# Kernel tuning notes

Measured on AMD Instinct MI355X. Metric: run time of the kernel, lower is better.

The kernel has to match this reference:

```python
import jax, jax.numpy as jnp
import numpy as np
from jax import lax

NPOINT = 1024
NSAMPLE = 32
RADIUS = 0.6
BN_EPS = 1e-5


def square_distance(src, dst):
    # src (B,S,3), dst (B,N,3) -> (B,S,N) squared distances
    d = -2.0 * jnp.einsum('bsc,bnc->bsn', src, dst)
    d = d + jnp.sum(src ** 2, -1)[:, :, None]
    d = d + jnp.sum(dst ** 2, -1)[:, None, :]
    return d


def farthest_point_sample(xyz, npoint):
    B, N, _ = xyz.shape
    bidx = jnp.arange(B)

    def step(carry, _):
        distance, farthest = carry
        centroid = xyz[bidx, farthest]                      # (B,3)
        dist = jnp.sum((xyz - centroid[:, None, :]) ** 2, -1)  # (B,N)
        distance = jnp.minimum(distance, dist)
        new_far = jnp.argmax(distance, -1)
        return (distance, new_far), farthest

    init = (jnp.full((B, N), 1e10, xyz.dtype), jnp.zeros((B,), jnp.int32))
    _, idxs = lax.scan(step, init, None, length=npoint)
    return idxs.T                                            # (B,npoint)


def ball_query(xyz, new_xyz, radius, nsample):
    B, N, _ = xyz.shape
    sqr = square_distance(new_xyz, xyz)                      # (B,S,N)
    idx = jnp.where(sqr <= radius ** 2, jnp.arange(N)[None, None, :], N)
    idx = jnp.sort(idx, axis=-1)[:, :, :nsample]             # (B,S,K)
    first = idx[:, :, :1]
    return jnp.where(idx == N, first, idx)


def gather2(points, idx):
    # points (B,N,C), idx (B,S) -> (B,S,C)
    return jax.vmap(lambda p, i: p[i])(points, idx)


def gather3(points, idx):
    # points (B,N,C), idx (B,S,K) -> (B,S,K,C)
    return jax.vmap(lambda p, i: p[i])(points, idx)


def sa_forward(xyz, features, params):
    fps_idx = lax.stop_gradient(farthest_point_sample(xyz, NPOINT))
    new_xyz = gather2(xyz, fps_idx)                          # (B,S,3)
    idx = lax.stop_gradient(ball_query(xyz, new_xyz, RADIUS, NSAMPLE))
    grouped_xyz = gather3(xyz, idx) - new_xyz[:, :, None, :] # (B,S,K,3)
    grouped_feat = gather3(features.transpose(0, 2, 1), idx) # (B,S,K,C)
    g = jnp.concatenate([grouped_xyz, grouped_feat], -1)     # (B,S,K,C+3)
    g = g.transpose(0, 3, 2, 1)                              # (B,Cin,K,S)
    for w, b, ga, be in params:
        g = jnp.einsum('oc,bcks->boks', w, g) + b[None, :, None, None]
        mu = jnp.mean(g, axis=(0, 2, 3), keepdims=True)
        var = jnp.var(g, axis=(0, 2, 3), keepdims=True)
        g = ga[None, :, None, None] * (g - mu) * lax.rsqrt(var + BN_EPS) \
            + be[None, :, None, None]
        g = jax.nn.relu(g)
    new_features = jnp.max(g, axis=2)                        # (B,Cout,S)
    return new_xyz, new_features


def setup_inputs() -> dict:
    key = jax.random.key(0)
    ks = jax.random.split(key, 8)
    B, N, C = 16, 4096, 128
    cin = C + 3
    mlp = [128, 128, 256]
    inp = {
        'xyz': jax.random.normal(ks[0], (B, N, 3), jnp.float32),
        'features': jax.random.normal(ks[1], (B, C, N), jnp.float32),
    }
    prev = cin
    for i, out in enumerate(mlp):
        inp[f'w{i}'] = jax.random.normal(ks[2 + i], (out, prev), jnp.float32) * 0.05
        inp[f'b{i}'] = jnp.zeros((out,), jnp.float32)
        inp[f'gamma{i}'] = jnp.ones((out,), jnp.float32)
        inp[f'beta{i}'] = jnp.zeros((out,), jnp.float32)
        prev = out
    return inp


def reference(xyz, features, w0, b0, gamma0, beta0, w1, b1, gamma1, beta1,
              w2, b2, gamma2, beta2):
    params = [(w0, b0, gamma0, beta0), (w1, b1, gamma1, beta1),
              (w2, b2, gamma2, beta2)]
    return sa_forward(xyz, features, params)
```

## Files before the change

### kernel.cpp

```cpp
#include <hip/hip_runtime.h>

#define B_ 16
#define N_ 4096
#define S_ 1024
#define K_ 32
#define PITCH2 136
#define PITCH1 168

typedef unsigned long long u64;
typedef short bf16x8 __attribute__((ext_vector_type(8)));
typedef unsigned short u16x8 __attribute__((ext_vector_type(8)));
typedef float f32x4 __attribute__((ext_vector_type(4)));
typedef float f32x2 __attribute__((ext_vector_type(2)));

__device__ __forceinline__ unsigned short f2bf(float f) {
  unsigned u = __float_as_uint(f);
  unsigned r = (u + 0x7FFFu + ((u >> 16) & 1u)) >> 16;
  return (unsigned short)r;
}
__device__ __forceinline__ float bf2f(unsigned short h) {
  return __uint_as_float(((unsigned)h) << 16);
}

#define DPP_MAX(v, ctrl)                                                        \
  {                                                                             \
    int _t = __builtin_amdgcn_update_dpp(__float_as_int(v), __float_as_int(v),  \
                                         ctrl, 0xf, 0xf, false);                \
    v = fmaxf(v, __int_as_float(_t));                                           \
  }

__global__ __launch_bounds__(512) void k_front(
    const float* __restrict__ xyz, float* __restrict__ new_xyz,
    const float* __restrict__ feat, unsigned short* __restrict__ featT,
    const float* __restrict__ w0, const float* __restrict__ w1,
    const float* __restrict__ w2, unsigned short* __restrict__ wbf0,
    unsigned short* __restrict__ wbf1, unsigned short* __restrict__ wbf2,
    float* __restrict__ stats) {
  __shared__ __align__(16) float smem[N_ * 4 + S_ + 64];
  int blk = blockIdx.x, t = threadIdx.x;

  if (blk < 16) {
#pragma clang fp contract(off)
#if __has_builtin(__builtin_amdgcn_s_setprio)
    __builtin_amdgcn_s_setprio(3);
#endif
    float4* pts = (float4*)smem;
    int* idxs = (int*)(smem + N_ * 4);
    u64* swk = (u64*)(smem + N_ * 4 + S_);
    int b = blk;
    const float* base = xyz + (size_t)b * N_ * 3;
    for (int i = t; i < N_; i += 512)
      pts[i] = make_float4(base[i * 3], base[i * 3 + 1], base[i * 3 + 2], 0.0f);
    if (t == 0) idxs[0] = 0;
    __syncthreads();
    f32x2 px[4], py[4], pz[4], pd[4];
    int i0 = t * 8;
    #pragma unroll
    for (int j = 0; j < 4; ++j) {
      float4 p0 = pts[i0 + 2 * j], p1 = pts[i0 + 2 * j + 1];
      px[j] = (f32x2){p0.x, p1.x};
      py[j] = (f32x2){p0.y, p1.y};
      pz[j] = (f32x2){p0.z, p1.z};
      pd[j] = (f32x2){1e10f, 1e10f};
    }
    int cur = 0;
    for (int it = 0; it < S_; ++it) {
      float4 c = pts[cur];
      f32x2 c2x = (f32x2){c.x, c.x}, c2y = (f32x2){c.y, c.y}, c2z = (f32x2){c.z, c.z};
      float bestv = -1.0f; int besti = 0;
      #pragma unroll
      for (int j = 0; j < 4; ++j) {
        f32x2 dx = px[j] - c2x;
        f32x2 dy = py[j] - c2y;
        f32x2 dz = pz[j] - c2z;
        f32x2 d = (dx * dx + dy * dy) + dz * dz;
        f32x2 dm = __builtin_elementwise_min(pd[j], d);
        pd[j] = dm;
        if (dm.x > bestv) { bestv = dm.x; besti = 2 * j; }
        if (dm.y > bestv) { bestv = dm.y; besti = 2 * j + 1; }
      }
      float v = bestv;
      DPP_MAX(v, 0x111);
      DPP_MAX(v, 0x112);
      DPP_MAX(v, 0x114);
      DPP_MAX(v, 0x118);
      DPP_MAX(v, 0x142);
      DPP_MAX(v, 0x143);
      float wmax = __int_as_float(__builtin_amdgcn_readlane(__float_as_int(v), 63));
      u64 mask = __ballot(bestv == wmax);
      int owner = __ffsll((long long)mask) - 1;
      int widx = __builtin_amdgcn_readlane(i0 + besti, owner);
      if ((t & 63) == 0)
        swk[(it & 1) * 8 + (t >> 6)] =
            ((u64)__float_as_uint(wmax) << 32) | (unsigned)(4095 - widx);
      __syncthreads();
      const u64* kk = swk + (it & 1) * 8;
      u64 k0 = kk[0];
      #pragma unroll
      for (int w = 1; w < 8; ++w) if (kk[w] > k0) k0 = kk[w];
      cur = 4095 - (int)(unsigned)(k0 & 0xFFFFFFFFull);
      if (t == 0 && it + 1 < S_) idxs[it + 1] = cur;
    }
    __syncthreads();
    for (int i = t; i < S_; i += 512) {
      float4 v = pts[idxs[i]];
      size_t o = ((size_t)b * S_ + i) * 3;
      new_xyz[o] = v.x; new_xyz[o + 1] = v.y; new_xyz[o + 2] = v.z;
    }
  } else if (blk < 32) {
    int id = (blk - 16) * 512 + t;
    const int st = 16 * 512;
    for (int i = id; i < 32768; i += st) stats[i] = 0.0f;
    for (int i = id; i < 128 * 160; i += st) {
      int n = i / 160, k = i - n * 160;
      float v = (k < 128) ? w0[n * 131 + 3 + k] : (k < 131) ? w0[n * 131 + k - 128] : 0.0f;
      wbf0[i] = f2bf(v);
    }
    for (int i = id; i < 128 * 128; i += st) wbf1[i] = f2bf(w1[i]);
    for (int i = id; i < 256 * 128; i += st) wbf2[i] = f2bf(w2[i]);
  } else {
    float (*tile)[33] = (float(*)[33])smem;
    int blk2 = blk - 32;
    int n0 = (blk2 & 127) * 32;
    int c0 = ((blk2 >> 7) & 3) * 32;
    int b = blk2 >> 9;
    int tx = t & 31, ty = t >> 5;
    #pragma unroll
    for (int j = 0; j < 32; j += 16)
      tile[ty + j][tx] = feat[((size_t)b * 128 + c0 + ty + j) * N_ + n0 + tx];
    __syncthreads();
    #pragma unroll
    for (int j = 0; j < 32; j += 16)
      featT[((size_t)b * N_ + n0 + ty + j) * 128 + c0 + tx] = f2bf(tile[tx][ty + j]);
  }
}

__global__ __launch_bounds__(256) void k_ballq(const float* __restrict__ xyz,
                                               const float* __restrict__ new_xyz,
                                               int* __restrict__ ball_idx) {
  int b = blockIdx.y;
  int s = blockIdx.x * 4 + (threadIdx.x >> 6);
  int lane = threadIdx.x & 63;
  const float* pb = xyz + (size_t)b * N_ * 3;
  size_t q = (size_t)b * S_ + s;
  float qx = new_xyz[q * 3], qy = new_xyz[q * 3 + 1], qz = new_xyz[q * 3 + 2];
  float sq = __fadd_rn(__fadd_rn(__fmul_rn(qx, qx), __fmul_rn(qy, qy)), __fmul_rn(qz, qz));
  int* out = ball_idx + q * K_;
  int total = 0;
  int first_idx = -1;
  for (int basei = 0; basei < N_; basei += 64) {
    int i = basei + lane;
    float fx = pb[i * 3], fy = pb[i * 3 + 1], fz = pb[i * 3 + 2];
    float dot = __fmul_rn(qx, fx);
    dot = __fadd_rn(dot, __fmul_rn(qy, fy));
    dot = __fadd_rn(dot, __fmul_rn(qz, fz));
    float sd = __fadd_rn(__fadd_rn(__fmul_rn(fx, fx), __fmul_rn(fy, fy)), __fmul_rn(fz, fz));
    float dist = __fadd_rn(__fadd_rn(__fmul_rn(-2.0f, dot), sq), sd);
    bool within = (dist <= 0.36f);
    u64 m = __ballot(within);
    if (first_idx < 0 && m) first_idx = basei + __ffsll((long long)m) - 1;
    if (within) {
      int pos = total + __popcll(m & ((1ull << lane) - 1ull));
      if (pos < K_) out[pos] = i;
    }
    total += (int)__popcll(m);
    if (total >= K_) break;
  }
  if (total < K_) {
    int k2 = total + lane;
    if (k2 < K_) out[k2] = first_idx;
  }
}

#define MFMA(a, b, c) __builtin_amdgcn_mfma_f32_16x16x32_bf16(a, b, c, 0, 0, 0)

__global__ __launch_bounds__(256) void k_layer1(
    const float* __restrict__ xyz, const float* __restrict__ new_xyz,
    const unsigned short* __restrict__ featT, const int* __restrict__ ball_idx,
    const unsigned short* __restrict__ wbf0, const float* __restrict__ b0,
    unsigned short* __restrict__ y, float* __restrict__ stats) {
  __shared__ __align__(16) unsigned short Wl[128 * PITCH1];
  __shared__ float sbias[128];
  int bb = blockIdx.y, s0 = blockIdx.x * 4, t = threadIdx.x;
  int w = t >> 6, L = t & 63, lm = L & 15, lg = L >> 4;
  size_t qg = (size_t)bb * S_ + s0 + w;

  int p0 = ball_idx[qg * K_ + lm];
  int p1 = ball_idx[qg * K_ + 16 + lm];
  const unsigned short* f0 = featT + ((size_t)bb * N_ + p0) * 128;
  const unsigned short* f1 = featT + ((size_t)bb * N_ + p1) * 128;
  bf16x8 a0[5], a1[5];
  #pragma unroll
  for (int kt = 0; kt < 4; ++kt) {
    a0[kt] = *(const bf16x8*)(f0 + kt * 32 + lg * 8);
    a1[kt] = *(const bf16x8*)(f1 + kt * 32 + lg * 8);
  }
  a0[4] = (bf16x8){0, 0, 0, 0, 0, 0, 0, 0};
  a1[4] = (bf16x8){0, 0, 0, 0, 0, 0, 0, 0};
  if (lg == 0) {
    float nx = new_xyz[qg * 3], ny = new_xyz[qg * 3 + 1], nz = new_xyz[qg * 3 + 2];
    const float* pp0 = xyz + ((size_t)bb * N_ + p0) * 3;
    const float* pp1 = xyz + ((size_t)bb * N_ + p1) * 3;
    a0[4][0] = (short)f2bf(pp0[0] - nx);
    a0[4][1] = (short)f2bf(pp0[1] - ny);
    a0[4][2] = (short)f2bf(pp0[2] - nz);
    a1[4][0] = (short)f2bf(pp1[0] - nx);
    a1[4][1] = (short)f2bf(pp1[1] - ny);
    a1[4][2] = (short)f2bf(pp1[2] - nz);
  }
  {
    int n = t >> 1, h = t & 1;
    const uint4* wr = (const uint4*)(wbf0 + n * 160 + h * 80);
    uint4* wl = (uint4*)(Wl + n * PITCH1 + h * 80);
    #pragma unroll
    for (int i = 0; i < 10; ++i) wl[i] = wr[i];
    if (t < 128) sbias[t] = b0[t];
  }
  __syncthreads();
  f32x4 acc[2][8];
  #pragma unroll
  for (int mi = 0; mi < 2; ++mi)
    #pragma unroll
    for (int nt = 0; nt < 8; ++nt) acc[mi][nt] = (f32x4){0.f, 0.f, 0.f, 0.f};
  #pragma unroll
  for (int kt = 0; kt < 5; ++kt) {
    int ko = kt * 32 + lg * 8;
    bf16x8 bv[8];
    #pragma unroll
    for (int nt = 0; nt < 8; ++nt)
      bv[nt] = *(const bf16x8*)&Wl[(nt * 16 + lm) * PITCH1 + ko];
    #pragma unroll
    for (int nt = 0; nt < 8; ++nt) {
      acc[0][nt] = MFMA(a0[kt], bv[nt], acc[0][nt]);
      acc[1][nt] = MFMA(a1[kt], bv[nt], acc[1][nt]);
    }
  }
  int slot = blockIdx.x & 31;
  #pragma unroll
  for (int nt = 0; nt < 8; ++nt) {
    int col = nt * 16 + lm;
    float bo = sbias[col];
    float s1 = 0.f, s2 = 0.f;
    #pragma unroll
    for (int mi = 0; mi < 2; ++mi)
      #pragma unroll
      for (int r = 0; r < 4; ++r) {
        float yv = acc[mi][nt][r] + bo;
        s1 += yv; s2 += yv * yv;
        int ks = mi * 16 + lg * 4 + r;
        y[(qg * K_ + ks) * 128 + col] = f2bf(yv);
      }
    s1 += __shfl_xor(s1, 16); s2 += __shfl_xor(s2, 16);
    s1 += __shfl_xor(s1, 32); s2 += __shfl_xor(s2, 32);
    if (lg == 0) {
      atomicAdd(stats + ((size_t)slot * 128 + col) * 2, s1);
      atomicAdd(stats + ((size_t)slot * 128 + col) * 2 + 1, s2);
    }
  }
}

__global__ __launch_bounds__(256) void k_layer2(
    unsigned short* y, const float* __restrict__ stats,
    const float* __restrict__ gamma, const float* __restrict__ beta,
    const unsigned short* __restrict__ wbf1, const float* __restrict__ b1,
    float* __restrict__ stats2) {
  __shared__ __align__(16) unsigned short Wl[128 * PITCH2];
  __shared__ __align__(16) float sa[128], sd[128];
  __shared__ float sbias[128];
  int bb = blockIdx.y, s0 = blockIdx.x * 4, t = threadIdx.x;
  int w = t >> 6, L = t & 63, lm = L & 15, lg = L >> 4;
  size_t qg = (size_t)bb * S_ + s0 + w;

  const u16x8* yr0 = (const u16x8*)(y + (qg * K_ + lm) * 128);
  const u16x8* yr1 = (const u16x8*)(y + (qg * K_ + 16 + lm) * 128);
  u16x8 raw0[4], raw1[4];
  #pragma unroll
  for (int kt = 0; kt < 4; ++kt) { raw0[kt] = yr0[kt * 4 + lg]; raw1[kt] = yr1[kt * 4 + lg]; }

  if (t < 128) {
    float s1 = 0.0f, s2 = 0.0f;
    for (int sl = 0; sl < 32; ++sl) {
      s1 += stats[((size_t)sl * 128 + t) * 2];
      s2 += stats[((size_t)sl * 128 + t) * 2 + 1];
    }
    const float inv = 1.0f / 524288.0f;
    float mu = s1 * inv;
    float var = s2 * inv - mu * mu;
    float a = gamma[t] * rsqrtf(var + 1e-5f);
    sa[t] = a;
    sd[t] = beta[t] - a * mu;
    sbias[t] = b1[t];
  }
  {
    int n = t >> 1, h = t & 1;
    const uint4* wr = (const uint4*)(wbf1 + n * 128 + h * 64);
    uint4* wl = (uint4*)(Wl + n * PITCH2 + h * 64);
    #pragma unroll
    for (int i = 0; i < 8; ++i) wl[i] = wr[i];
  }
  __syncthreads();
  bf16x8 a0[4], a1[4];
  #pragma unroll
  for (int kt = 0; kt < 4; ++kt) {
    int c = kt * 32 + lg * 8;
    f32x4 A0 = *(const f32x4*)&sa[c], A1 = *(const f32x4*)&sa[c + 4];
    f32x4 D0 = *(const f32x4*)&sd[c], D1 = *(const f32x4*)&sd[c + 4];
    #pragma unroll
    for (int j = 0; j < 4; ++j) {
      a0[kt][j]     = (short)f2bf(fmaxf(A0[j] * bf2f(raw0[kt][j])     + D0[j], 0.f));
      a0[kt][j + 4] = (short)f2bf(fmaxf(A1[j] * bf2f(raw0[kt][j + 4]) + D1[j], 0.f));
      a1[kt][j]     = (short)f2bf(fmaxf(A0[j] * bf2f(raw1[kt][j])     + D0[j], 0.f));
      a1[kt][j + 4] = (short)f2bf(fmaxf(A1[j] * bf2f(raw1[kt][j + 4]) + D1[j], 0.f));
    }
  }
  f32x4 acc[2][8];
  #pragma unroll
  for (int mi = 0; mi < 2; ++mi)
    #pragma unroll
    for (int nt = 0; nt < 8; ++nt) acc[mi][nt] = (f32x4){0.f, 0.f, 0.f, 0.f};
  #pragma unroll
  for (int kt = 0; kt < 4; ++kt) {
    int ko = kt * 32 + lg * 8;
    bf16x8 bv[8];
    #pragma unroll
    for (int nt = 0; nt < 8; ++nt)
      bv[nt] = *(const bf16x8*)&Wl[(nt * 16 + lm) * PITCH2 + ko];
    #pragma unroll
    for (int nt = 0; nt < 8; ++nt) {
      acc[0][nt] = MFMA(a0[kt], bv[nt], acc[0][nt]);
      acc[1][nt] = MFMA(a1[kt], bv[nt], acc[1][nt]);
    }
  }
  int slot = blockIdx.x & 31;
  #pragma unroll
  for (int nt = 0; nt < 8; ++nt) {
    int col = nt * 16 + lm;
    float bo = sbias[col];
    float s1 = 0.f, s2 = 0.f;
    #pragma unroll
    for (int mi = 0; mi < 2; ++mi)
      #pragma unroll
      for (int r = 0; r < 4; ++r) {
        float yv = acc[mi][nt][r] + bo;
        s1 += yv; s2 += yv * yv;
        int ks = mi * 16 + lg * 4 + r;
        y[(qg * K_ + ks) * 128 + col] = f2bf(yv);
      }
    s1 += __shfl_xor(s1, 16); s2 += __shfl_xor(s2, 16);
    s1 += __shfl_xor(s1, 32); s2 += __shfl_xor(s2, 32);
    if (lg == 0) {
      atomicAdd(stats2 + ((size_t)slot * 128 + col) * 2, s1);
      atomicAdd(stats2 + ((size_t)slot * 128 + col) * 2 + 1, s2);
    }
  }
}

__global__ __launch_bounds__(256) void k_layer3(
    const unsigned short* __restrict__ y, const float* __restrict__ stats2,
    const float* __restrict__ gamma, const float* __restrict__ beta,
    const unsigned short* __restrict__ wbf2, const float* __restrict__ b2,
    unsigned short* __restrict__ ymax, unsigned short* __restrict__ ymin,
    float* __restrict__ stats3) {
  __shared__ __align__(16) unsigned short Wl[128 * PITCH2];
  __shared__ __align__(16) float sa[128], sd[128];
  __shared__ float sbias[128];
  int bb = blockIdx.y, s0 = blockIdx.x * 4, nh = blockIdx.z, t = threadIdx.x;
  int w = t >> 6, L = t & 63, lm = L & 15, lg = L >> 4;
  size_t qg = (size_t)bb * S_ + s0 + w;

  const u16x8* yr0 = (const u16x8*)(y + (qg * K_ + lm) * 128);
  const u16x8* yr1 = (const u16x8*)(y + (qg * K_ + 16 + lm) * 128);
  u16x8 raw0[4], raw1[4];
  #pragma unroll
  for (int kt = 0; kt < 4; ++kt) { raw0[kt] = yr0[kt * 4 + lg]; raw1[kt] = yr1[kt * 4 + lg]; }

  if (t < 128) {
    float s1 = 0.0f, s2 = 0.0f;
    for (int sl = 0; sl < 32; ++sl) {
      s1 += stats2[((size_t)sl * 128 + t) * 2];
      s2 += stats2[((size_t)sl * 128 + t) * 2 + 1];
    }
    const float inv = 1.0f / 524288.0f;
    float mu = s1 * inv;
    float var = s2 * inv - mu * mu;
    float a = gamma[t] * rsqrtf(var + 1e-5f);
    sa[t] = a;
    sd[t] = beta[t] - a * mu;
    sbias[t] = b2[nh * 128 + t];
  }
  {
    int n = t >> 1, h = t & 1;
    const uint4* wr = (const uint4*)(wbf2 + (size_t)(nh * 128 + n) * 128 + h * 64);
    uint4* wl = (uint4*)(Wl + n * PITCH2 + h * 64);
    #pragma unroll
    for (int i = 0; i < 8; ++i) wl[i] = wr[i];
  }
  __syncthreads();
  bf16x8 a0[4], a1[4];
  #pragma unroll
  for (int kt = 0; kt < 4; ++kt) {
    int c = kt * 32 + lg * 8;
    f32x4 A0 = *(const f32x4*)&sa[c], A1 = *(const f32x4*)&sa[c + 4];
    f32x4 D0 = *(const f32x4*)&sd[c], D1 = *(const f32x4*)&sd[c + 4];
    #pragma unroll
    for (int j = 0; j < 4; ++j) {
      a0[kt][j]     = (short)f2bf(fmaxf(A0[j] * bf2f(raw0[kt][j])     + D0[j], 0.f));
      a0[kt][j + 4] = (short)f2bf(fmaxf(A1[j] * bf2f(raw0[kt][j + 4]) + D1[j], 0.f));
      a1[kt][j]     = (short)f2bf(fmaxf(A0[j] * bf2f(raw1[kt][j])     + D0[j], 0.f));
      a1[kt][j + 4] = (short)f2bf(fmaxf(A1[j] * bf2f(raw1[kt][j + 4]) + D1[j], 0.f));
    }
  }
  f32x4 acc[2][8];
  #pragma unroll
  for (int mi = 0; mi < 2; ++mi)
    #pragma unroll
    for (int nt = 0; nt < 8; ++nt) acc[mi][nt] = (f32x4){0.f, 0.f, 0.f, 0.f};
  #pragma unroll
  for (int kt = 0; kt < 4; ++kt) {
    int ko = kt * 32 + lg * 8;
    bf16x8 bv[8];
    #pragma unroll
    for (int nt = 0; nt < 8; ++nt)
      bv[nt] = *(const bf16x8*)&Wl[(nt * 16 + lm) * PITCH2 + ko];
    #pragma unroll
    for (int nt = 0; nt < 8; ++nt) {
      acc[0][nt] = MFMA(a0[kt], bv[nt], acc[0][nt]);
      acc[1][nt] = MFMA(a1[kt], bv[nt], acc[1][nt]);
    }
  }
  int slot = blockIdx.x & 31;
  #pragma unroll
  for (int nt = 0; nt < 8; ++nt) {
    int col = nt * 16 + lm;
    int o = nh * 128 + col;
    float bo = sbias[col];
    float s1 = 0.f, s2 = 0.f, mx = -3.4e38f, mn = 3.4e38f;
    #pragma unroll
    for (int mi = 0; mi < 2; ++mi)
      #pragma unroll
      for (int r = 0; r < 4; ++r) {
        float yv = acc[mi][nt][r] + bo;
        s1 += yv; s2 += yv * yv;
        mx = fmaxf(mx, yv); mn = fminf(mn, yv);
      }
    s1 += __shfl_xor(s1, 16); s2 += __shfl_xor(s2, 16);
    s1 += __shfl_xor(s1, 32); s2 += __shfl_xor(s2, 32);
    mx = fmaxf(mx, __shfl_xor(mx, 16)); mx = fmaxf(mx, __shfl_xor(mx, 32));
    mn = fminf(mn, __shfl_xor(mn, 16)); mn = fminf(mn, __shfl_xor(mn, 32));
    if (lg == 0) {
      ymax[qg * 256 + o] = f2bf(mx);
      ymin[qg * 256 + o] = f2bf(mn);
      atomicAdd(stats3 + ((size_t)slot * 256 + o) * 2, s1);
      atomicAdd(stats3 + ((size_t)slot * 256 + o) * 2 + 1, s2);
    }
  }
}

__global__ __launch_bounds__(256) void k_final(const unsigned short* __restrict__ ymax,
                                               const unsigned short* __restrict__ ymin,
                                               const float* __restrict__ stats3,
                                               const float* __restrict__ gamma,
                                               const float* __restrict__ beta,
                                               float* __restrict__ out2) {
  __shared__ float tile[32][33];
  __shared__ float smA[32], smD[32];
  int b = blockIdx.z, o0 = blockIdx.y * 32, s0 = blockIdx.x * 32;
  int tx = threadIdx.x, ty = threadIdx.y;
  if (ty == 0) {
    int c = o0 + tx;
    float s1 = 0.0f, s2 = 0.0f;
    for (int sl = 0; sl < 32; ++sl) {
      s1 += stats3[((size_t)sl * 256 + c) * 2];
      s2 += stats3[((size_t)sl * 256 + c) * 2 + 1];
    }
    const float inv = 1.0f / 524288.0f;
    float mu = s1 * inv;
    float var = s2 * inv - mu * mu;
    float a = gamma[c] * rsqrtf(var + 1e-5f);
    smA[tx] = a;
    smD[tx] = beta[c] - a * mu;
  }
  __syncthreads();
  float a_rd = smA[tx];
  #pragma unroll
  for (int j = 0; j < 32; j += 8) {
    size_t src = ((size_t)b * S_ + s0 + ty + j) * 256 + o0 + tx;
    tile[ty + j][tx] = (a_rd >= 0.0f) ? bf2f(ymax[src]) : bf2f(ymin[src]);
  }
  __syncthreads();
  #pragma unroll
  for (int j = 0; j < 32; j += 8) {
    float a = smA[ty + j], dd = smD[ty + j];
    out2[((size_t)b * 256 + o0 + ty + j) * S_ + s0 + tx] = fmaxf(a * tile[tx][ty + j] + dd, 0.0f);
  }
}

extern "C" void kernel_launch(void* const* d_in, const int* in_sizes, int n_in,
                              void* d_out, int out_size, void* d_ws, size_t ws_size,
                              hipStream_t stream) {
  (void)in_sizes; (void)n_in; (void)out_size; (void)ws_size;
  const float* xyz  = (const float*)d_in[0];
  const float* feat = (const float*)d_in[1];
  const float* w0   = (const float*)d_in[2];
  const float* b0   = (const float*)d_in[3];
  const float* ga0  = (const float*)d_in[4];
  const float* be0  = (const float*)d_in[5];
  const float* w1   = (const float*)d_in[6];
  const float* b1   = (const float*)d_in[7];
  const float* ga1  = (const float*)d_in[8];
  const float* be1  = (const float*)d_in[9];
  const float* w2   = (const float*)d_in[10];
  const float* b2   = (const float*)d_in[11];
  const float* ga2  = (const float*)d_in[12];
  const float* be2  = (const float*)d_in[13];

  float* out_xyz  = (float*)d_out;
  float* out_feat = out_xyz + (size_t)B_ * S_ * 3;

  char* ws = (char*)d_ws;
  size_t off = 0;
  auto alloc = [&](size_t bytes) -> void* {
    void* p = ws + off;
    off += (bytes + 255) & ~(size_t)255;
    return p;
  };
  unsigned short* featT = (unsigned short*)alloc((size_t)B_ * N_ * 128 * 2);
  int*   ball  = (int*)alloc((size_t)B_ * S_ * K_ * 4);
  float* stats = (float*)alloc(32768 * 4);
  unsigned short* wbf0 = (unsigned short*)alloc(128 * 160 * 2);
  unsigned short* wbf1 = (unsigned short*)alloc(128 * 128 * 2);
  unsigned short* wbf2 = (unsigned short*)alloc(256 * 128 * 2);
  unsigned short* ymaxb = (unsigned short*)alloc((size_t)B_ * S_ * 256 * 2);
  unsigned short* yminb = (unsigned short*)alloc((size_t)B_ * S_ * 256 * 2);
  unsigned short* y = (unsigned short*)alloc((size_t)B_ * S_ * K_ * 128 * 2);

  k_front<<<16 + 16 + 8192, 512, 0, stream>>>(xyz, out_xyz, feat, featT,
                                              w0, w1, w2, wbf0, wbf1, wbf2, stats);
  k_ballq<<<dim3(256, 16), 256, 0, stream>>>(xyz, out_xyz, ball);
  k_layer1<<<dim3(256, 16), 256, 0, stream>>>(xyz, out_xyz, featT, ball, wbf0, b0, y, stats);
  k_layer2<<<dim3(256, 16), 256, 0, stream>>>(y, stats, ga0, be0, wbf1, b1, stats + 8192);
  k_layer3<<<dim3(256, 16, 2), 256, 0, stream>>>(y, stats + 8192, ga1, be1, wbf2, b2,
                                                 ymaxb, yminb, stats + 16384);
  k_final<<<dim3(32, 8, 16), dim3(32, 8), 0, stream>>>(ymaxb, yminb, stats + 16384,
                                                       ga2, be2, out_feat);
}
```

Measured before the change: 1.133 ms.

## Make MLP layer kernels persistent to amortize weight staging across tiles

The three MLP layer kernels become grid-stride persistent loops over 4096 tiles, launched with 768, 1024 and 512x2 blocks instead of one block per tile. Each block loads the bf16 weight matrix into LDS, and computes the BN scale/shift from the 32 stat slots, once, then reuses them for several tiles. This removes the repeated per-tile weight copy and stats reduction. The cost is fewer blocks in flight and no overlap between one tile's global loads and the previous tile's MFMA work.

```diff
diff --git a/kernel.cpp b/kernel.cpp
--- a/kernel.cpp
+++ b/kernel.cpp
@@ -173,6 +173,7 @@
 }
 
 #define MFMA(a, b, c) __builtin_amdgcn_mfma_f32_16x16x32_bf16(a, b, c, 0, 0, 0)
+#define NTILES 4096
 
 __global__ __launch_bounds__(256) void k_layer1(
     const float* __restrict__ xyz, const float* __restrict__ new_xyz,
@@ -181,33 +182,8 @@
     unsigned short* __restrict__ y, float* __restrict__ stats) {
   __shared__ __align__(16) unsigned short Wl[128 * PITCH1];
   __shared__ float sbias[128];
-  int bb = blockIdx.y, s0 = blockIdx.x * 4, t = threadIdx.x;
+  int t = threadIdx.x;
   int w = t >> 6, L = t & 63, lm = L & 15, lg = L >> 4;
-  size_t qg = (size_t)bb * S_ + s0 + w;
-
-  int p0 = ball_idx[qg * K_ + lm];
-  int p1 = ball_idx[qg * K_ + 16 + lm];
-  const unsigned short* f0 = featT + ((size_t)bb * N_ + p0) * 128;
-  const unsigned short* f1 = featT + ((size_t)bb * N_ + p1) * 128;
-  bf16x8 a0[5], a1[5];
-  #pragma unroll
-  for (int kt = 0; kt < 4; ++kt) {
-    a0[kt] = *(const bf16x8*)(f0 + kt * 32 + lg * 8);
-    a1[kt] = *(const bf16x8*)(f1 + kt * 32 + lg * 8);
-  }
-  a0[4] = (bf16x8){0, 0, 0, 0, 0, 0, 0, 0};
-  a1[4] = (bf16x8){0, 0, 0, 0, 0, 0, 0, 0};
-  if (lg == 0) {
-    float nx = new_xyz[qg * 3], ny = new_xyz[qg * 3 + 1], nz = new_xyz[qg * 3 + 2];
-    const float* pp0 = xyz + ((size_t)bb * N_ + p0) * 3;
-    const float* pp1 = xyz + ((size_t)bb * N_ + p1) * 3;
-    a0[4][0] = (short)f2bf(pp0[0] - nx);
-    a0[4][1] = (short)f2bf(pp0[1] - ny);
-    a0[4][2] = (short)f2bf(pp0[2] - nz);
-    a1[4][0] = (short)f2bf(pp1[0] - nx);
-    a1[4][1] = (short)f2bf(pp1[1] - ny);
-    a1[4][2] = (short)f2bf(pp1[2] - nz);
-  }
   {
     int n = t >> 1, h = t & 1;
     const uint4* wr = (const uint4*)(wbf0 + n * 160 + h * 80);
@@ -217,44 +193,74 @@
     if (t < 128) sbias[t] = b0[t];
   }
   __syncthreads();
-  f32x4 acc[2][8];
-  #pragma unroll
-  for (int mi = 0; mi < 2; ++mi)
-    #pragma unroll
-    for (int nt = 0; nt < 8; ++nt) acc[mi][nt] = (f32x4){0.f, 0.f, 0.f, 0.f};
-  #pragma unroll
-  for (int kt = 0; kt < 5; ++kt) {
-    int ko = kt * 32 + lg * 8;
-    bf16x8 bv[8];
-    #pragma unroll
-    for (int nt = 0; nt < 8; ++nt)
-      bv[nt] = *(const bf16x8*)&Wl[(nt * 16 + lm) * PITCH1 + ko];
+
+  for (int tile = blockIdx.x; tile < NTILES; tile += gridDim.x) {
+    int bb = tile >> 8;
+    int s0 = (tile & 255) * 4;
+    size_t qg = (size_t)bb * S_ + s0 + w;
+
+    int p0 = ball_idx[qg * K_ + lm];
+    int p1 = ball_idx[qg * K_ + 16 + lm];
+    const unsigned short* f0 = featT + ((size_t)bb * N_ + p0) * 128;
+    const unsigned short* f1 = featT + ((size_t)bb * N_ + p1) * 128;
+    bf16x8 a0[5], a1[5];
+    #pragma unroll
+    for (int kt = 0; kt < 4; ++kt) {
+      a0[kt] = *(const bf16x8*)(f0 + kt * 32 + lg * 8);
+      a1[kt] = *(const bf16x8*)(f1 + kt * 32 + lg * 8);
+    }
+    a0[4] = (bf16x8){0, 0, 0, 0, 0, 0, 0, 0};
+    a1[4] = (bf16x8){0, 0, 0, 0, 0, 0, 0, 0};
+    if (lg == 0) {
+      float nx = new_xyz[qg * 3], ny = new_xyz[qg * 3 + 1], nz = new_xyz[qg * 3 + 2];
+      const float* pp0 = xyz + ((size_t)bb * N_ + p0) * 3;
+      const float* pp1 = xyz + ((size_t)bb * N_ + p1) * 3;
+      a0[4][0] = (short)f2bf(pp0[0] - nx);
+      a0[4][1] = (short)f2bf(pp0[1] - ny);
+      a0[4][2] = (short)f2bf(pp0[2] - nz);
+      a1[4][0] = (short)f2bf(pp1[0] - nx);
+      a1[4][1] = (short)f2bf(pp1[1] - ny);
+      a1[4][2] = (short)f2bf(pp1[2] - nz);
+    }
+    f32x4 acc[2][8];
+    #pragma unroll
+    for (int mi = 0; mi < 2; ++mi)
+      #pragma unroll
+      for (int nt = 0; nt < 8; ++nt) acc[mi][nt] = (f32x4){0.f, 0.f, 0.f, 0.f};
+    #pragma unroll
+    for (int kt = 0; kt < 5; ++kt) {
+      int ko = kt * 32 + lg * 8;
+      bf16x8 bv[8];
+      #pragma unroll
+      for (int nt = 0; nt < 8; ++nt)
+        bv[nt] = *(const bf16x8*)&Wl[(nt * 16 + lm) * PITCH1 + ko];
+      #pragma unroll
+      for (int nt = 0; nt < 8; ++nt) {
+        acc[0][nt] = MFMA(a0[kt], bv[nt], acc[0][nt]);
+        acc[1][nt] = MFMA(a1[kt], bv[nt], acc[1][nt]);
+      }
+    }
+    int slot = tile & 31;
     #pragma unroll
     for (int nt = 0; nt < 8; ++nt) {
-      acc[0][nt] = MFMA(a0[kt], bv[nt], acc[0][nt]);
-      acc[1][nt] = MFMA(a1[kt], bv[nt], acc[1][nt]);
-    }
-  }
-  int slot = blockIdx.x & 31;
-  #pragma unroll
-  for (int nt = 0; nt < 8; ++nt) {
-    int col = nt * 16 + lm;
-    float bo = sbias[col];
-    float s1 = 0.f, s2 = 0.f;
-    #pragma unroll
-    for (int mi = 0; mi < 2; ++mi)
-      #pragma unroll
-      for (int r = 0; r < 4; ++r) {
-        float yv = acc[mi][nt][r] + bo;
-        s1 += yv; s2 += yv * yv;
-        int ks = mi * 16 + lg * 4 + r;
-        y[(qg * K_ + ks) * 128 + col] = f2bf(yv);
-      }
-    s1 += __shfl_xor(s1, 16); s2 += __shfl_xor(s2, 16);
-    s1 += __shfl_xor(s1, 32); s2 += __shfl_xor(s2, 32);
-    if (lg == 0) {
-      atomicAdd(stats + ((size_t)slot * 128 + col) * 2, s1);
-      atomicAdd(stats + ((size_t)slot * 128 + col) * 2 + 1, s2);
+      int col = nt * 16 + lm;
+      float bo = sbias[col];
+      float s1 = 0.f, s2 = 0.f;
+      #pragma unroll
+      for (int mi = 0; mi < 2; ++mi)
+        #pragma unroll
+        for (int r = 0; r < 4; ++r) {
+          float yv = acc[mi][nt][r] + bo;
+          s1 += yv; s2 += yv * yv;
+          int ks = mi * 16 + lg * 4 + r;
+          y[(qg * K_ + ks) * 128 + col] = f2bf(yv);
+        }
+      s1 += __shfl_xor(s1, 16); s2 += __shfl_xor(s2, 16);
+      s1 += __shfl_xor(s1, 32); s2 += __shfl_xor(s2, 32);
+      if (lg == 0) {
+        atomicAdd(stats + ((size_t)slot * 128 + col) * 2, s1);
+        atomicAdd(stats + ((size_t)slot * 128 + col) * 2 + 1, s2);
+      }
     }
   }
 }
@@ -267,16 +273,8 @@
   __shared__ __align__(16) unsigned short Wl[128 * PITCH2];
   __shared__ __align__(16) float sa[128], sd[128];
   __shared__ float sbias[128];
-  int bb = blockIdx.y, s0 = blockIdx.x * 4, t = threadIdx.x;
+  int t = threadIdx.x;
   int w = t >> 6, L = t & 63, lm = L & 15, lg = L >> 4;
-  size_t qg = (size_t)bb * S_ + s0 + w;
-
-  const u16x8* yr0 = (const u16x8*)(y + (qg * K_ + lm) * 128);
-  const u16x8* yr1 = (const u16x8*)(y + (qg * K_ + 16 + lm) * 128);
-  u16x8 raw0[4], raw1[4];
-  #pragma unroll
-  for (int kt = 0; kt < 4; ++kt) { raw0[kt] = yr0[kt * 4 + lg]; raw1[kt] = yr1[kt * 4 + lg]; }
-
   if (t < 128) {
     float s1 = 0.0f, s2 = 0.0f;
     for (int sl = 0; sl < 32; ++sl) {
@@ -299,58 +297,70 @@
     for (int i = 0; i < 8; ++i) wl[i] = wr[i];
   }
   __syncthreads();
-  bf16x8 a0[4], a1[4];
-  #pragma unroll
-  for (int kt = 0; kt < 4; ++kt) {
-    int c = kt * 32 + lg * 8;
-    f32x4 A0 = *(const f32x4*)&sa[c], A1 = *(const f32x4*)&sa[c + 4];
-    f32x4 D0 = *(const f32x4*)&sd[c], D1 = *(const f32x4*)&sd[c + 4];
-    #pragma unroll
-    for (int j = 0; j < 4; ++j) {
-      a0[kt][j]     = (short)f2bf(fmaxf(A0[j] * bf2f(raw0[kt][j])     + D0[j], 0.f));
-      a0[kt][j + 4] = (short)f2bf(fmaxf(A1[j] * bf2f(raw0[kt][j + 4]) + D1[j], 0.f));
-      a1[kt][j]     = (short)f2bf(fmaxf(A0[j] * bf2f(raw1[kt][j])     + D0[j], 0.f));
-      a1[kt][j + 4] = (short)f2bf(fmaxf(A1[j] * bf2f(raw1[kt][j + 4]) + D1[j], 0.f));
-    }
-  }
-  f32x4 acc[2][8];
-  #pragma unroll
-  for (int mi = 0; mi < 2; ++mi)
-    #pragma unroll
-    for (int nt = 0; nt < 8; ++nt) acc[mi][nt] = (f32x4){0.f, 0.f, 0.f, 0.f};
-  #pragma unroll
-  for (int kt = 0; kt < 4; ++kt) {
-    int ko = kt * 32 + lg * 8;
-    bf16x8 bv[8];
-    #pragma unroll
-    for (int nt = 0; nt < 8; ++nt)
-      bv[nt] = *(const bf16x8*)&Wl[(nt * 16 + lm) * PITCH2 + ko];
+
+  for (int tile = blockIdx.x; tile < NTILES; tile += gridDim.x) {
+    int bb = tile >> 8;
+    int s0 = (tile & 255) * 4;
+    size_t qg = (size_t)bb * S_ + s0 + w;
+
+    const u16x8* yr0 = (const u16x8*)(y + (qg * K_ + lm) * 128);
+    const u16x8* yr1 = (const u16x8*)(y + (qg * K_ + 16 + lm) * 128);
+    u16x8 raw0[4], raw1[4];
+    #pragma unroll
+    for (int kt = 0; kt < 4; ++kt) { raw0[kt] = yr0[kt * 4 + lg]; raw1[kt] = yr1[kt * 4 + lg]; }
+    bf16x8 a0[4], a1[4];
+    #pragma unroll
+    for (int kt = 0; kt < 4; ++kt) {
+      int c = kt * 32 + lg * 8;
+      f32x4 A0 = *(const f32x4*)&sa[c], A1 = *(const f32x4*)&sa[c + 4];
+      f32x4 D0 = *(const f32x4*)&sd[c], D1 = *(const f32x4*)&sd[c + 4];
+      #pragma unroll
+      for (int j = 0; j < 4; ++j) {
+        a0[kt][j]     = (short)f2bf(fmaxf(A0[j] * bf2f(raw0[kt][j])     + D0[j], 0.f));
+        a0[kt][j + 4] = (short)f2bf(fmaxf(A1[j] * bf2f(raw0[kt][j + 4]) + D1[j], 0.f));
+        a1[kt][j]     = (short)f2bf(fmaxf(A0[j] * bf2f(raw1[kt][j])     + D0[j], 0.f));
+        a1[kt][j + 4] = (short)f2bf(fmaxf(A1[j] * bf2f(raw1[kt][j + 4]) + D1[j], 0.f));
+      }
+    }
+    f32x4 acc[2][8];
+    #pragma unroll
+    for (int mi = 0; mi < 2; ++mi)
+      #pragma unroll
+      for (int nt = 0; nt < 8; ++nt) acc[mi][nt] = (f32x4){0.f, 0.f, 0.f, 0.f};
+    #pragma unroll
+    for (int kt = 0; kt < 4; ++kt) {
+      int ko = kt * 32 + lg * 8;
+      bf16x8 bv[8];
+      #pragma unroll
+      for (int nt = 0; nt < 8; ++nt)
+        bv[nt] = *(const bf16x8*)&Wl[(nt * 16 + lm) * PITCH2 + ko];
+      #pragma unroll
+      for (int nt = 0; nt < 8; ++nt) {
+        acc[0][nt] = MFMA(a0[kt], bv[nt], acc[0][nt]);
+        acc[1][nt] = MFMA(a1[kt], bv[nt], acc[1][nt]);
+      }
+    }
+    int slot = tile & 31;
     #pragma unroll
     for (int nt = 0; nt < 8; ++nt) {
-      acc[0][nt] = MFMA(a0[kt], bv[nt], acc[0][nt]);
-      acc[1][nt] = MFMA(a1[kt], bv[nt], acc[1][nt]);
-    }
-  }
-  int slot = blockIdx.x & 31;
-  #pragma unroll
-  for (int nt = 0; nt < 8; ++nt) {
-    int col = nt * 16 + lm;
-    float bo = sbias[col];
-    float s1 = 0.f, s2 = 0.f;
-    #pragma unroll
-    for (int mi = 0; mi < 2; ++mi)
-      #pragma unroll
-      for (int r = 0; r < 4; ++r) {
-        float yv = acc[mi][nt][r] + bo;
-        s1 += yv; s2 += yv * yv;
-        int ks = mi * 16 + lg * 4 + r;
-        y[(qg * K_ + ks) * 128 + col] = f2bf(yv);
-      }
-    s1 += __shfl_xor(s1, 16); s2 += __shfl_xor(s2, 16);
-    s1 += __shfl_xor(s1, 32); s2 += __shfl_xor(s2, 32);
-    if (lg == 0) {
-      atomicAdd(stats2 + ((size_t)slot * 128 + col) * 2, s1);
-      atomicAdd(stats2 + ((size_t)slot * 128 + col) * 2 + 1, s2);
+      int col = nt * 16 + lm;
+      float bo = sbias[col];
+      float s1 = 0.f, s2 = 0.f;
+      #pragma unroll
+      for (int mi = 0; mi < 2; ++mi)
+        #pragma unroll
+        for (int r = 0; r < 4; ++r) {
+          float yv = acc[mi][nt][r] + bo;
+          s1 += yv; s2 += yv * yv;
+          int ks = mi * 16 + lg * 4 + r;
+          y[(qg * K_ + ks) * 128 + col] = f2bf(yv);
+        }
+      s1 += __shfl_xor(s1, 16); s2 += __shfl_xor(s2, 16);
+      s1 += __shfl_xor(s1, 32); s2 += __shfl_xor(s2, 32);
+      if (lg == 0) {
+        atomicAdd(stats2 + ((size_t)slot * 128 + col) * 2, s1);
+        atomicAdd(stats2 + ((size_t)slot * 128 + col) * 2 + 1, s2);
+      }
     }
   }
 }
@@ -364,16 +374,8 @@
   __shared__ __align__(16) unsigned short Wl[128 * PITCH2];
   __shared__ __align__(16) float sa[128], sd[128];
   __shared__ float sbias[128];
-  int bb = blockIdx.y, s0 = blockIdx.x * 4, nh = blockIdx.z, t = threadIdx.x;
+  int nh = blockIdx.y, t = threadIdx.x;
   int w = t >> 6, L = t & 63, lm = L & 15, lg = L >> 4;
-  size_t qg = (size_t)bb * S_ + s0 + w;
-
-  const u16x8* yr0 = (const u16x8*)(y + (qg * K_ + lm) * 128);
-  const u16x8* yr1 = (const u16x8*)(y + (qg * K_ + 16 + lm) * 128);
-  u16x8 raw0[4], raw1[4];
-  #pragma unroll
-  for (int kt = 0; kt < 4; ++kt) { raw0[kt] = yr0[kt * 4 + lg]; raw1[kt] = yr1[kt * 4 + lg]; }
-
   if (t < 128) {
     float s1 = 0.0f, s2 = 0.0f;
     for (int sl = 0; sl < 32; ++sl) {
@@ -396,62 +398,74 @@
     for (int i = 0; i < 8; ++i) wl[i] = wr[i];
   }
   __syncthreads();
-  bf16x8 a0[4], a1[4];
-  #pragma unroll
-  for (int kt = 0; kt < 4; ++kt) {
-    int c = kt * 32 + lg * 8;
-    f32x4 A0 = *(const f32x4*)&sa[c], A1 = *(const f32x4*)&sa[c + 4];
-    f32x4 D0 = *(const f32x4*)&sd[c], D1 = *(const f32x4*)&sd[c + 4];
-    #pragma unroll
-    for (int j = 0; j < 4; ++j) {
-      a0[kt][j]     = (short)f2bf(fmaxf(A0[j] * bf2f(raw0[kt][j])     + D0[j], 0.f));
-      a0[kt][j + 4] = (short)f2bf(fmaxf(A1[j] * bf2f(raw0[kt][j + 4]) + D1[j], 0.f));
-      a1[kt][j]     = (short)f2bf(fmaxf(A0[j] * bf2f(raw1[kt][j])     + D0[j], 0.f));
-      a1[kt][j + 4] = (short)f2bf(fmaxf(A1[j] * bf2f(raw1[kt][j + 4]) + D1[j], 0.f));
-    }
-  }
-  f32x4 acc[2][8];
-  #pragma unroll
-  for (int mi = 0; mi < 2; ++mi)
-    #pragma unroll
-    for (int nt = 0; nt < 8; ++nt) acc[mi][nt] = (f32x4){0.f, 0.f, 0.f, 0.f};
-  #pragma unroll
-  for (int kt = 0; kt < 4; ++kt) {
-    int ko = kt * 32 + lg * 8;
-    bf16x8 bv[8];
-    #pragma unroll
-    for (int nt = 0; nt < 8; ++nt)
-      bv[nt] = *(const bf16x8*)&Wl[(nt * 16 + lm) * PITCH2 + ko];
+
+  for (int tile = blockIdx.x; tile < NTILES; tile += gridDim.x) {
+    int bb = tile >> 8;
+    int s0 = (tile & 255) * 4;
+    size_t qg = (size_t)bb * S_ + s0 + w;
+
+    const u16x8* yr0 = (const u16x8*)(y + (qg * K_ + lm) * 128);
+    const u16x8* yr1 = (const u16x8*)(y + (qg * K_ + 16 + lm) * 128);
+    u16x8 raw0[4], raw1[4];
+    #pragma unroll
+    for (int kt = 0; kt < 4; ++kt) { raw0[kt] = yr0[kt * 4 + lg]; raw1[kt] = yr1[kt * 4 + lg]; }
+    bf16x8 a0[4], a1[4];
+    #pragma unroll
+    for (int kt = 0; kt < 4; ++kt) {
+      int c = kt * 32 + lg * 8;
+      f32x4 A0 = *(const f32x4*)&sa[c], A1 = *(const f32x4*)&sa[c + 4];
+      f32x4 D0 = *(const f32x4*)&sd[c], D1 = *(const f32x4*)&sd[c + 4];
+      #pragma unroll
+      for (int j = 0; j < 4; ++j) {
+        a0[kt][j]     = (short)f2bf(fmaxf(A0[j] * bf2f(raw0[kt][j])     + D0[j], 0.f));
+        a0[kt][j + 4] = (short)f2bf(fmaxf(A1[j] * bf2f(raw0[kt][j + 4]) + D1[j], 0.f));
+        a1[kt][j]     = (short)f2bf(fmaxf(A0[j] * bf2f(raw1[kt][j])     + D0[j], 0.f));
+        a1[kt][j + 4] = (short)f2bf(fmaxf(A1[j] * bf2f(raw1[kt][j + 4]) + D1[j], 0.f));
+      }
+    }
+    f32x4 acc[2][8];
+    #pragma unroll
+    for (int mi = 0; mi < 2; ++mi)
+      #pragma unroll
+      for (int nt = 0; nt < 8; ++nt) acc[mi][nt] = (f32x4){0.f, 0.f, 0.f, 0.f};
+    #pragma unroll
+    for (int kt = 0; kt < 4; ++kt) {
+      int ko = kt * 32 + lg * 8;
+      bf16x8 bv[8];
+      #pragma unroll
+      for (int nt = 0; nt < 8; ++nt)
+        bv[nt] = *(const bf16x8*)&Wl[(nt * 16 + lm) * PITCH2 + ko];
+      #pragma unroll
+      for (int nt = 0; nt < 8; ++nt) {
+        acc[0][nt] = MFMA(a0[kt], bv[nt], acc[0][nt]);
+        acc[1][nt] = MFMA(a1[kt], bv[nt], acc[1][nt]);
+      }
+    }
+    int slot = tile & 31;
     #pragma unroll
     for (int nt = 0; nt < 8; ++nt) {
-      acc[0][nt] = MFMA(a0[kt], bv[nt], acc[0][nt]);
-      acc[1][nt] = MFMA(a1[kt], bv[nt], acc[1][nt]);
-    }
-  }
-  int slot = blockIdx.x & 31;
-  #pragma unroll
-  for (int nt = 0; nt < 8; ++nt) {
-    int col = nt * 16 + lm;
-    int o = nh * 128 + col;
-    float bo = sbias[col];
-    float s1 = 0.f, s2 = 0.f, mx = -3.4e38f, mn = 3.4e38f;
-    #pragma unroll
-    for (int mi = 0; mi < 2; ++mi)
-      #pragma unroll
-      for (int r = 0; r < 4; ++r) {
-        float yv = acc[mi][nt][r] + bo;
-        s1 += yv; s2 += yv * yv;
-        mx = fmaxf(mx, yv); mn = fminf(mn, yv);
-      }
-    s1 += __shfl_xor(s1, 16); s2 += __shfl_xor(s2, 16);
-    s1 += __shfl_xor(s1, 32); s2 += __shfl_xor(s2, 32);
-    mx = fmaxf(mx, __shfl_xor(mx, 16)); mx = fmaxf(mx, __shfl_xor(mx, 32));
-    mn = fminf(mn, __shfl_xor(mn, 16)); mn = fminf(mn, __shfl_xor(mn, 32));
-    if (lg == 0) {
-      ymax[qg * 256 + o] = f2bf(mx);
-      ymin[qg * 256 + o] = f2bf(mn);
-      atomicAdd(stats3 + ((size_t)slot * 256 + o) * 2, s1);
-      atomicAdd(stats3 + ((size_t)slot * 256 + o) * 2 + 1, s2);
+      int col = nt * 16 + lm;
+      int o = nh * 128 + col;
+      float bo = sbias[col];
+      float s1 = 0.f, s2 = 0.f, mx = -3.4e38f, mn = 3.4e38f;
+      #pragma unroll
+      for (int mi = 0; mi < 2; ++mi)
+        #pragma unroll
+        for (int r = 0; r < 4; ++r) {
+          float yv = acc[mi][nt][r] + bo;
+          s1 += yv; s2 += yv * yv;
+          mx = fmaxf(mx, yv); mn = fminf(mn, yv);
+        }
+      s1 += __shfl_xor(s1, 16); s2 += __shfl_xor(s2, 16);
+      s1 += __shfl_xor(s1, 32); s2 += __shfl_xor(s2, 32);
+      mx = fmaxf(mx, __shfl_xor(mx, 16)); mx = fmaxf(mx, __shfl_xor(mx, 32));
+      mn = fminf(mn, __shfl_xor(mn, 16)); mn = fminf(mn, __shfl_xor(mn, 32));
+      if (lg == 0) {
+        ymax[qg * 256 + o] = f2bf(mx);
+        ymin[qg * 256 + o] = f2bf(mn);
+        atomicAdd(stats3 + ((size_t)slot * 256 + o) * 2, s1);
+        atomicAdd(stats3 + ((size_t)slot * 256 + o) * 2 + 1, s2);
+      }
     }
   }
 }
@@ -537,10 +551,10 @@
   k_front<<<16 + 16 + 8192, 512, 0, stream>>>(xyz, out_xyz, feat, featT,
                                               w0, w1, w2, wbf0, wbf1, wbf2, stats);
   k_ballq<<<dim3(256, 16), 256, 0, stream>>>(xyz, out_xyz, ball);
-  k_layer1<<<dim3(256, 16), 256, 0, stream>>>(xyz, out_xyz, featT, ball, wbf0, b0, y, stats);
-  k_layer2<<<dim3(256, 16), 256, 0, stream>>>(y, stats, ga0, be0, wbf1, b1, stats + 8192);
-  k_layer3<<<dim3(256, 16, 2), 256, 0, stream>>>(y, stats + 8192, ga1, be1, wbf2, b2,
-                                                 ymaxb, yminb, stats + 16384);
+  k_layer1<<<768, 256, 0, stream>>>(xyz, out_xyz, featT, ball, wbf0, b0, y, stats);
+  k_layer2<<<1024, 256, 0, stream>>>(y, stats, ga0, be0, wbf1, b1, stats + 8192);
+  k_layer3<<<dim3(512, 2), 256, 0, stream>>>(y, stats + 8192, ga1, be1, wbf2, b2,
+                                             ymaxb, yminb, stats + 16384);
   k_final<<<dim3(32, 8, 16), dim3(32, 8), 0, stream>>>(ymaxb, yminb, stats + 16384,
                                                        ga2, be2, out_feat);
 }
```

Measured after the change: 1.084 ms. -4.3%, faster.
